# Kernel tuning notes

Hardware: AMD Instinct MI355X
Metric: run time of the kernel (lower is better)

## Reference

```python
import jax, jax.numpy as jnp
import numpy as np

N_NODES = 100000


def gcn_conv(x, W, b, src, dst, n_nodes):
    """PyG-style GCNConv: out = D^{-1/2} (A + I) D^{-1/2} (x @ W) + b."""
    h = x @ W  # [N, F_out] transform first (smaller message dim)
    # add self-loops
    loops = jnp.arange(n_nodes, dtype=src.dtype)
    s = jnp.concatenate([src, loops])
    d = jnp.concatenate([dst, loops])
    # symmetric normalization
    deg = jnp.zeros((n_nodes,), dtype=h.dtype).at[d].add(1.0)
    dinv = jnp.where(deg > 0, jax.lax.rsqrt(deg), 0.0)
    norm = dinv[s] * dinv[d]  # [E+N]
    msg = h[s] * norm[:, None]  # gather from sources
    out = jax.ops.segment_sum(msg, d, num_segments=n_nodes)  # scatter-add at targets
    return out + b


def setup_inputs() -> dict:
    key = jax.random.key(0)
    k1, k2, k3, k4 = jax.random.split(key, 4)
    in_ch, hid, out_ch = 128, 75, 40
    n_edges = 3200000
    x = jax.random.normal(k1, (N_NODES, in_ch), dtype=jnp.float32)
    edge_index = jax.random.randint(k2, (2, n_edges), 0, N_NODES, dtype=jnp.int64)
    # Glorot-style init for GCNConv weights, zero bias (PyG default)
    W1 = jax.random.normal(k3, (in_ch, hid), dtype=jnp.float32) * (1.0 / np.sqrt(in_ch))
    b1 = jnp.zeros((hid,), dtype=jnp.float32)
    W2 = jax.random.normal(k4, (hid, out_ch), dtype=jnp.float32) * (1.0 / np.sqrt(hid))
    b2 = jnp.zeros((out_ch,), dtype=jnp.float32)
    return {"x": x, "edge_index": edge_index, "W1": W1, "b1": b1, "W2": W2, "b2": b2}


def reference(x, edge_index, W1, b1, W2, b2):
    src, dst = edge_index[0], edge_index[1]
    h = gcn_conv(x, W1, b1, src, dst, N_NODES)
    h = jax.nn.relu(h)
    h = gcn_conv(h, W2, b2, src, dst, N_NODES)
    return jax.nn.log_softmax(h, axis=1)
```

## Files before the change

kernel.cpp:

```cpp
#include <hip/hip_runtime.h>

#define N_NODES 100000
#define IN_CH 128
#define HID 75
#define OUT_CH 40
#define N_EDGES 3200000

#define NB 196
#define CAP 20000
#define EPT 16
#define PA_EDGES (EPT * 256)

typedef unsigned short u16;
typedef unsigned int u32;
typedef unsigned char u8;
typedef short short8 __attribute__((ext_vector_type(8)));
typedef float f32x4 __attribute__((ext_vector_type(4)));
typedef float f32x2 __attribute__((ext_vector_type(2)));
typedef u32 u32x2 __attribute__((ext_vector_type(2)));
typedef u32 u32x4 __attribute__((ext_vector_type(4)));

__device__ __forceinline__ u16 f2bf(float f) {
    u32 b = __float_as_uint(f);
    b += 0x7FFF + ((b >> 16) & 1);
    return (u16)(b >> 16);
}

#if __has_builtin(__builtin_amdgcn_cvt_pk_f32_fp8) && __has_builtin(__builtin_amdgcn_cvt_pk_fp8_f32)
#define HW_FP8 1
#else
#define HW_FP8 0
#endif

__device__ __forceinline__ float dec1_sw(u32 v) {
    u32 s = (v & 0x80u) << 24;
    u32 em = v & 0x7Fu;
    float mag = (em >= 8u) ? __uint_as_float((em << 20) + (120u << 23))
                           : (float)em * 0.001953125f;
    return __uint_as_float(s | __float_as_uint(mag));
}
template <int HI>
__device__ __forceinline__ f32x2 dec2(u32 w) {
#if HW_FP8
    return __builtin_amdgcn_cvt_pk_f32_fp8(w, HI);
#else
    f32x2 r;
    r.x = dec1_sw((w >> (HI * 16)) & 0xFFu);
    r.y = dec1_sw((w >> (HI * 16 + 8)) & 0xFFu);
    return r;
#endif
}
__device__ __forceinline__ u32 enc1(float f) {
#if HW_FP8
    return __builtin_amdgcn_cvt_pk_fp8_f32(f, f, 0u, false) & 0xFFu;
#else
    float cf = fminf(fmaxf(f, -448.f), 448.f);
    u32 b = __float_as_uint(cf);
    u32 sign = (b >> 24) & 0x80u;
    float af = fabsf(cf);
    if (af < 0.015625f) {
        u32 d = (u32)__builtin_rintf(af * 512.f);
        return sign | d;
    }
    u32 e = (b >> 23) & 0xFFu;
    u32 m = b & 0x7FFFFFu;
    u32 m8 = m >> 20;
    u32 rem = m & 0xFFFFFu;
    m8 += (rem > 0x80000u) || (rem == 0x80000u && (m8 & 1u));
    u32 ee = e - 120u;
    if (m8 == 8u) { m8 = 0u; ee += 1u; }
    if (ee > 15u || (ee == 15u && m8 == 7u)) { ee = 15u; m8 = 6u; }
    return sign | (ee << 3) | m8;
#endif
}

__global__ void probe64(const int* __restrict__ e, int* __restrict__ flag) {
    __shared__ int nonzero;
    if (threadIdx.x == 0) nonzero = 0;
    __syncthreads();
    int idx = threadIdx.x * 12497;
    if (e[2 * idx + 1] != 0) nonzero = 1;
    __syncthreads();
    if (threadIdx.x == 0) *flag = (nonzero == 0) ? 1 : 0;
}

__global__ __launch_bounds__(256) void init_misc(int* __restrict__ bucketCursor,
        u32* __restrict__ h1b32) {
    int i = blockIdx.x * 256 + threadIdx.x;
    if (i < NB * 16) bucketCursor[i] = 0;
    if (i < 800000) {
        int node = i >> 3, q = i & 7;
        h1b32[node * 48 + 40 + q] = 0;
    }
}

__global__ __launch_bounds__(256) void passA(const int* __restrict__ e,
        const int* __restrict__ flag, int* __restrict__ bucketCursor,
        unsigned* __restrict__ bucketBuf) {
    __shared__ int cnt[NB];
    __shared__ int base[NB];
    int t = threadIdx.x;
    for (int i = t; i < NB; i += 256) cnt[i] = 0;
    __syncthreads();
    bool w64 = (*flag != 0);
    int s_[EPT], d_[EPT];
    int eb = blockIdx.x * PA_EDGES + t;
#pragma unroll
    for (int k = 0; k < EPT; ++k) {
        int idx = eb + k * 256;
        int s = 0, d = -1;
        if (idx < N_EDGES) {
            if (w64) { s = e[2 * idx]; d = e[2 * (N_EDGES + idx)]; }
            else     { s = e[idx];     d = e[N_EDGES + idx]; }
            atomicAdd(&cnt[d >> 9], 1);
        }
        s_[k] = s; d_[k] = d;
    }
    __syncthreads();
    for (int i = t; i < NB; i += 256) {
        int c = cnt[i];
        base[i] = (c > 0) ? atomicAdd(&bucketCursor[i * 16], c) : 0;
        cnt[i] = 0;
    }
    __syncthreads();
#pragma unroll
    for (int k = 0; k < EPT; ++k) {
        int d = d_[k];
        if (d >= 0) {
            int b = d >> 9;
            int off = atomicAdd(&cnt[b], 1);
            int pos = base[b] + off;
            if (pos < CAP)
                bucketBuf[(size_t)b * CAP + pos] =
                    ((unsigned)(d & 511) << 17) | (unsigned)s_[k];
        }
    }
}

__global__ __launch_bounds__(256) void scan196(const int* __restrict__ bucketCursor,
        int* __restrict__ bucketStart, int* __restrict__ rowStart) {
    __shared__ int a[256], b[256];
    int t = threadIdx.x;
    int v = (t < NB) ? bucketCursor[t * 16] : 0;
    a[t] = v;
    __syncthreads();
    int* pin = a; int* pout = b;
    for (int o = 1; o < 256; o <<= 1) {
        int nv = pin[t] + ((t >= o) ? pin[t - o] : 0);
        pout[t] = nv;
        __syncthreads();
        int* tmp = pin; pin = pout; pout = tmp;
    }
    if (t < NB) bucketStart[t] = pin[t] - v;
    if (t == 0) rowStart[N_NODES] = N_EDGES;
}

__global__ __launch_bounds__(1024) void passB(const unsigned* __restrict__ bucketBuf,
        const int* __restrict__ bucketCursor, const int* __restrict__ bucketStart,
        int* __restrict__ csrSrc, int* __restrict__ rowStart, float* __restrict__ dinv) {
    __shared__ int cnt[512];
    __shared__ int sa[512], sb[512];
    int b = blockIdx.x;
    int t = threadIdx.x;
    int n = bucketCursor[b * 16];
    int start = bucketStart[b];
    if (t < 512) cnt[t] = 0;
    __syncthreads();
    const unsigned* buf = bucketBuf + (size_t)b * CAP;
    for (int i = t; i < n; i += 1024) atomicAdd(&cnt[buf[i] >> 17], 1);
    __syncthreads();
    if (t < 512) sa[t] = cnt[t];
    __syncthreads();
    int* pin = sa; int* pout = sb;
    for (int o = 1; o < 512; o <<= 1) {
        if (t < 512) pout[t] = pin[t] + ((t >= o) ? pin[t - o] : 0);
        __syncthreads();
        int* tmp = pin; pin = pout; pout = tmp;
    }
    int excl = 0;
    if (t < 512) {
        int deg = cnt[t];
        excl = pin[t] - deg;
        int node = b * 512 + t;
        if (node < N_NODES) {
            rowStart[node] = start + excl;
            dinv[node] = rsqrtf((float)deg + 1.0f);
        }
    }
    __syncthreads();
    if (t < 512) cnt[t] = excl;
    __syncthreads();
    for (int i = t; i < n; i += 1024) {
        unsigned p = buf[i];
        int pos = atomicAdd(&cnt[p >> 17], 1);
        csrSrc[start + pos] = (int)(p & 0x1FFFF);
    }
}

__global__ __launch_bounds__(256) void prep_w(const float* __restrict__ W1,
        const float* __restrict__ W2, u16* __restrict__ w1t, u16* __restrict__ w2t) {
    int g = blockIdx.x * 256 + threadIdx.x;
    int stride = gridDim.x * 256;
    for (int i = g; i < 80 * 128; i += stride) {
        int c = i >> 7, k = i & 127;
        w1t[i] = (c < HID) ? f2bf(W1[k * HID + c]) : (u16)0;
    }
    for (int i = g; i < 48 * 96; i += stride) {
        int c = i / 96, k = i - c * 96;
        w2t[i] = (c < OUT_CH && k < HID) ? f2bf(W2[k * OUT_CH + c]) : (u16)0;
    }
}

__global__ __launch_bounds__(256) void gemm1_mfma(const float* __restrict__ x,
        const u16* __restrict__ w1t, const float* __restrict__ dinv,
        u8* __restrict__ hsA8, u8* __restrict__ hsB8) {
    __shared__ u16 Wl[80 * 136];
    int t = threadIdx.x;
    {
        const u32* ws = (const u32*)w1t;
        u32* wd = (u32*)Wl;
        for (int i = t; i < 80 * 64; i += 256) {
            int r = i >> 6, c = i & 63;
            wd[r * 68 + c] = ws[i];
        }
    }
    __syncthreads();
    int wid = t >> 6, lane = t & 63;
    int bl = lane & 15, kh = lane >> 4;
    int row0 = blockIdx.x * 64 + wid * 16;
    short8 bf[5][4];
#pragma unroll
    for (int ct = 0; ct < 5; ++ct)
#pragma unroll
        for (int ks = 0; ks < 4; ++ks)
            bf[ct][ks] = *(const short8*)&Wl[(ct * 16 + bl) * 136 + ks * 32 + kh * 8];
    f32x4 zero = {0.f, 0.f, 0.f, 0.f};
    f32x4 acc[5];
#pragma unroll
    for (int ct = 0; ct < 5; ++ct) acc[ct] = zero;
    int arow = row0 + bl;
    bool av = (arow < N_NODES);
    const float* xr = x + (size_t)arow * IN_CH + kh * 8;
#pragma unroll
    for (int ks = 0; ks < 4; ++ks) {
        short8 af = {0, 0, 0, 0, 0, 0, 0, 0};
        if (av) {
            float4 lo = *(const float4*)(xr + ks * 32);
            float4 hi = *(const float4*)(xr + ks * 32 + 4);
            af[0] = (short)f2bf(lo.x); af[1] = (short)f2bf(lo.y);
            af[2] = (short)f2bf(lo.z); af[3] = (short)f2bf(lo.w);
            af[4] = (short)f2bf(hi.x); af[5] = (short)f2bf(hi.y);
            af[6] = (short)f2bf(hi.z); af[7] = (short)f2bf(hi.w);
        }
#pragma unroll
        for (int ct = 0; ct < 5; ++ct)
            acc[ct] = __builtin_amdgcn_mfma_f32_16x16x32_bf16(af, bf[ct][ks], acc[ct], 0, 0, 0);
    }
    int orow = row0 + kh * 4;
    float dn[4];
#pragma unroll
    for (int i = 0; i < 4; ++i)
        dn[i] = (orow + i < N_NODES) ? dinv[orow + i] * 8.f : 0.f;
#pragma unroll
    for (int ct = 0; ct < 5; ++ct) {
        int col = ct * 16 + bl;
#pragma unroll
        for (int i = 0; i < 4; ++i) {
            int r = orow + i;
            if (r < N_NODES) {
                u8 q8 = (u8)enc1(acc[ct][i] * dn[i]);
                if (ct < 4) hsA8[(size_t)r * 64 + col] = q8;
                else        hsB8[(size_t)r * 16 + (col - 64)] = q8;
            }
        }
    }
}

__global__ __launch_bounds__(256) void gemm2_mfma(const u16* __restrict__ h1b,
        const u16* __restrict__ w2t, const float* __restrict__ dinv,
        u8* __restrict__ hs2A8, u8* __restrict__ hs2B8) {
    __shared__ u16 Wl[48 * 104];
    int t = threadIdx.x;
    {
        const u32* ws = (const u32*)w2t;
        u32* wd = (u32*)Wl;
        for (int i = t; i < 48 * 48; i += 256) {
            int r = i / 48, c = i - r * 48;
            wd[r * 52 + c] = ws[i];
        }
    }
    __syncthreads();
    int wid = t >> 6, lane = t & 63;
    int bl = lane & 15, kh = lane >> 4;
    int row0 = blockIdx.x * 64 + wid * 16;
    short8 bf[3][3];
#pragma unroll
    for (int ct = 0; ct < 3; ++ct)
#pragma unroll
        for (int ks = 0; ks < 3; ++ks)
            bf[ct][ks] = *(const short8*)&Wl[(ct * 16 + bl) * 104 + ks * 32 + kh * 8];
    f32x4 zero = {0.f, 0.f, 0.f, 0.f};
    f32x4 acc[3];
#pragma unroll
    for (int ct = 0; ct < 3; ++ct) acc[ct] = zero;
    int arow = row0 + bl;
    bool av = (arow < N_NODES);
    const u16* hr = h1b + (size_t)arow * 96 + kh * 8;
#pragma unroll
    for (int ks = 0; ks < 3; ++ks) {
        short8 af = {0, 0, 0, 0, 0, 0, 0, 0};
        if (av) af = *(const short8*)(hr + ks * 32);
#pragma unroll
        for (int ct = 0; ct < 3; ++ct)
            acc[ct] = __builtin_amdgcn_mfma_f32_16x16x32_bf16(af, bf[ct][ks], acc[ct], 0, 0, 0);
    }
    int orow = row0 + kh * 4;
    float dn[4];
#pragma unroll
    for (int i = 0; i < 4; ++i)
        dn[i] = (orow + i < N_NODES) ? dinv[orow + i] * 8.f : 0.f;
#pragma unroll
    for (int ct = 0; ct < 3; ++ct) {
        int col = ct * 16 + bl;
#pragma unroll
        for (int i = 0; i < 4; ++i) {
            int r = orow + i;
            if (r < N_NODES) {
                u8 q8 = (u8)enc1(acc[ct][i] * dn[i]);
                if (ct < 2)      hs2A8[(size_t)r * 32 + col] = q8;
                else if (bl < 8) hs2B8[(size_t)r * 8 + (col - 32)] = q8;
            }
        }
    }
}

__global__ __launch_bounds__(256) void aggregate1(
        const char* __restrict__ tab, int delta1,
        const int* __restrict__ rowStart, const int* __restrict__ csrSrc,
        const float* __restrict__ dinv, const float* __restrict__ bias,
        u32* __restrict__ out) {
    int wid = threadIdx.x >> 6, lane = threadIdx.x & 63;
    int node = __builtin_amdgcn_readfirstlane(blockIdx.x * 4 + wid);
    if (node >= N_NODES) return;
    int g = lane / 10;
    int ll = lane - 10 * g;
    bool isB = ll >= 8;
    u32 loff = isB ? (u32)(ll - 8) * 8 + (u32)delta1 : (u32)ll * 8;
    int sh = isB ? 4 : 6;
    bool act = lane < 60;
    f32x2 a0 = {0.f, 0.f}, a1 = {0.f, 0.f}, a2 = {0.f, 0.f}, a3 = {0.f, 0.f};
    if (lane < 10) {
        u32x2 v = *(const u32x2*)(tab + (((u32)node << sh) + loff));
        a0 += dec2<0>(v.x); a1 += dec2<1>(v.x);
        a2 += dec2<0>(v.y); a3 += dec2<1>(v.y);
    }
    int j = rowStart[node], end = rowStart[node + 1];
    for (; j + 24 <= end; j += 24) {
        u32 iv[4]; u32x2 vv[4];
#pragma unroll
        for (int q = 0; q < 4; ++q) iv[q] = act ? (u32)csrSrc[j + 6 * q + g] : 0u;
#pragma unroll
        for (int q = 0; q < 4; ++q) {
            u32x2 z = {0u, 0u};
            vv[q] = act ? *(const u32x2*)(tab + ((iv[q] << sh) + loff)) : z;
        }
#pragma unroll
        for (int q = 0; q < 4; ++q) {
            a0 += dec2<0>(vv[q].x); a1 += dec2<1>(vv[q].x);
            a2 += dec2<0>(vv[q].y); a3 += dec2<1>(vv[q].y);
        }
    }
    for (; j < end; j += 6) {
        bool p = act && (j + g < end);
        u32 ivx = p ? (u32)csrSrc[j + g] : 0u;
        u32x2 z = {0u, 0u};
        u32x2 v = p ? *(const u32x2*)(tab + ((ivx << sh) + loff)) : z;
        a0 += dec2<0>(v.x); a1 += dec2<1>(v.x);
        a2 += dec2<0>(v.y); a3 += dec2<1>(v.y);
    }
    float tt[8] = {a0.x, a0.y, a1.x, a1.y, a2.x, a2.y, a3.x, a3.y};
#pragma unroll
    for (int k = 0; k < 8; ++k) {
        tt[k] += __shfl(tt[k], lane + 30);
        tt[k] += __shfl(tt[k], lane + 10) + __shfl(tt[k], lane + 20);
    }
    if (lane < 10) {
        float dns = dinv[node] * 0.125f;
        u32x4 ov;
#pragma unroll
        for (int k = 0; k < 4; ++k) {
            int f0 = 8 * ll + 2 * k;
            float rlo = (f0 < HID) ? fmaxf(fmaf(dns, tt[2 * k], bias[f0]), 0.f) : 0.f;
            float rhi = (f0 + 1 < HID) ? fmaxf(fmaf(dns, tt[2 * k + 1], bias[f0 + 1]), 0.f) : 0.f;
            ov[k] = ((u32)f2bf(rhi) << 16) | (u32)f2bf(rlo);
        }
        *(u32x4*)(out + (size_t)node * 48 + 4 * ll) = ov;
    }
}

__global__ __launch_bounds__(256) void aggregate2(
        const char* __restrict__ tab, int delta2,
        const int* __restrict__ rowStart, const int* __restrict__ csrSrc,
        const float* __restrict__ dinv, const float* __restrict__ bias,
        float* __restrict__ out) {
    int wid = threadIdx.x >> 6, lane = threadIdx.x & 63;
    int node = __builtin_amdgcn_readfirstlane(blockIdx.x * 4 + wid);
    if (node >= N_NODES) return;
    int g = lane / 5;
    int ll = lane - 5 * g;
    bool isB = (ll == 4);
    u32 loff = isB ? (u32)delta2 : (u32)ll * 8;
    int sh = isB ? 3 : 5;
    bool act = lane < 60;
    f32x2 a0 = {0.f, 0.f}, a1 = {0.f, 0.f}, a2 = {0.f, 0.f}, a3 = {0.f, 0.f};
    if (lane < 5) {
        u32x2 v = *(const u32x2*)(tab + (((u32)node << sh) + loff));
        a0 += dec2<0>(v.x); a1 += dec2<1>(v.x);
        a2 += dec2<0>(v.y); a3 += dec2<1>(v.y);
    }
    int j = rowStart[node], end = rowStart[node + 1];
    for (; j + 24 <= end; j += 24) {
        u32 iv[2]; u32x2 vv[2];
#pragma unroll
        for (int q = 0; q < 2; ++q) iv[q] = act ? (u32)csrSrc[j + 12 * q + g] : 0u;
#pragma unroll
        for (int q = 0; q < 2; ++q) {
            u32x2 z = {0u, 0u};
            vv[q] = act ? *(const u32x2*)(tab + ((iv[q] << sh) + loff)) : z;
        }
#pragma unroll
        for (int q = 0; q < 2; ++q) {
            a0 += dec2<0>(vv[q].x); a1 += dec2<1>(vv[q].x);
            a2 += dec2<0>(vv[q].y); a3 += dec2<1>(vv[q].y);
        }
    }
    for (; j < end; j += 12) {
        bool p = act && (j + g < end);
        u32 ivx = p ? (u32)csrSrc[j + g] : 0u;
        u32x2 z = {0u, 0u};
        u32x2 v = p ? *(const u32x2*)(tab + ((ivx << sh) + loff)) : z;
        a0 += dec2<0>(v.x); a1 += dec2<1>(v.x);
        a2 += dec2<0>(v.y); a3 += dec2<1>(v.y);
    }
    float tt[8] = {a0.x, a0.y, a1.x, a1.y, a2.x, a2.y, a3.x, a3.y};
#pragma unroll
    for (int k = 0; k < 8; ++k) {
        tt[k] += __shfl(tt[k], lane + 30);
        tt[k] += __shfl(tt[k], lane + 10) + __shfl(tt[k], lane + 20);
        tt[k] += __shfl(tt[k], lane + 5);
    }
    bool act5 = lane < 5;
    float vk[8];
    float m = -3.4e38f;
    if (act5) {
        float dns = dinv[node] * 0.125f;
#pragma unroll
        for (int k = 0; k < 8; ++k) {
            vk[k] = fmaf(dns, tt[k], bias[8 * ll + k]);
            m = fmaxf(m, vk[k]);
        }
    }
#pragma unroll
    for (int o = 1; o < 8; o <<= 1) m = fmaxf(m, __shfl_xor(m, o));
    float e = 0.f;
    if (act5) {
#pragma unroll
        for (int k = 0; k < 8; ++k) e += expf(vk[k] - m);
    }
#pragma unroll
    for (int o = 1; o < 8; o <<= 1) e += __shfl_xor(e, o);
    float lse = logf(e);
    if (act5) {
        float4 r0 = make_float4(vk[0] - m - lse, vk[1] - m - lse,
                                vk[2] - m - lse, vk[3] - m - lse);
        float4 r1 = make_float4(vk[4] - m - lse, vk[5] - m - lse,
                                vk[6] - m - lse, vk[7] - m - lse);
        *(float4*)(out + (size_t)node * OUT_CH + 8 * ll) = r0;
        *(float4*)(out + (size_t)node * OUT_CH + 8 * ll + 4) = r1;
    }
}

extern "C" void kernel_launch(void* const* d_in, const int* in_sizes, int n_in,
                              void* d_out, int out_size, void* d_ws, size_t ws_size,
                              hipStream_t stream) {
    const float* x  = (const float*)d_in[0];
    const int*   e  = (const int*)d_in[1];
    const float* W1 = (const float*)d_in[2];
    const float* b1 = (const float*)d_in[3];
    const float* W2 = (const float*)d_in[4];
    const float* b2 = (const float*)d_in[5];
    float* out = (float*)d_out;

    char* w = (char*)d_ws;
    u8* hsA8 = (u8*)w;
    u8* hsB8 = (u8*)(w + 6402048);
    unsigned* bucketBuf = (unsigned*)w;
    w += 15680000;
    u16* h1b  = (u16*)w; w += (size_t)100032 * 96 * 2;
    int* csrSrc = (int*)w; w += (size_t)N_EDGES * 4;
    u8* hs2A8 = (u8*)w; w += (size_t)100032 * 32;
    u8* hs2B8 = (u8*)w; w += (size_t)100032 * 8;
    int* rowStart = (int*)w; w += 400016;
    float* dinv   = (float*)w; w += 400000;
    int* bucketCursor = (int*)w; w += NB * 16 * 4;
    int* bucketStart  = (int*)w; w += 1024;
    u16* w1t = (u16*)w; w += 80 * 128 * 2;
    u16* w2t = (u16*)w; w += 48 * 96 * 2;
    int* flag = (int*)w; w += 16;

    int delta1 = (int)((char*)hsB8 - (char*)hsA8);
    int delta2 = (int)((char*)hs2B8 - (char*)hs2A8);

    probe64<<<1, 256, 0, stream>>>(e, flag);
    init_misc<<<3126, 256, 0, stream>>>(bucketCursor, (u32*)h1b);
    passA<<<(N_EDGES + PA_EDGES - 1) / PA_EDGES, 256, 0, stream>>>(
        e, flag, bucketCursor, bucketBuf);
    scan196<<<1, 256, 0, stream>>>(bucketCursor, bucketStart, rowStart);
    passB<<<NB, 1024, 0, stream>>>(bucketBuf, bucketCursor, bucketStart,
                                   csrSrc, rowStart, dinv);
    prep_w<<<16, 256, 0, stream>>>(W1, W2, w1t, w2t);

    gemm1_mfma<<<(N_NODES + 63) / 64, 256, 0, stream>>>(x, w1t, dinv, hsA8, hsB8);
    aggregate1<<<(N_NODES + 3) / 4, 256, 0, stream>>>(
        (const char*)hsA8, delta1, rowStart, csrSrc, dinv, b1, (u32*)h1b);
    gemm2_mfma<<<(N_NODES + 63) / 64, 256, 0, stream>>>(h1b, w2t, dinv, hs2A8, hs2B8);
    aggregate2<<<(N_NODES + 3) / 4, 256, 0, stream>>>(
        (const char*)hs2A8, delta2, rowStart, csrSrc, dinv, b2, out);
}
```

Baseline: 264.4 us.

## Widen aggregate1 gathers to 16B and pad layer-2 table to 64B rows

aggregate1 now assigns 5 lanes per edge, each loading 16 bytes, so 12 edges are processed per wave step instead of 6 with 8-byte loads. The layer-2 quantized features move from a split A/B table into a single padded table with 64-byte rows, which removes the per-lane branch and delta offset in aggregate2. The goal is fewer memory instructions per gathered row and simpler addressing. In exchange the layer-2 table takes more memory footprint per node, and aggregate1 holds more accumulator registers.

```diff
diff --git a/kernel.cpp b/kernel.cpp
--- a/kernel.cpp
+++ b/kernel.cpp
@@ -278,7 +278,7 @@
 
 __global__ __launch_bounds__(256) void gemm2_mfma(const u16* __restrict__ h1b,
         const u16* __restrict__ w2t, const float* __restrict__ dinv,
-        u8* __restrict__ hs2A8, u8* __restrict__ hs2B8) {
+        u8* __restrict__ hs2P) {
     __shared__ u16 Wl[48 * 104];
     int t = threadIdx.x;
     {
@@ -325,10 +325,9 @@
 #pragma unroll
         for (int i = 0; i < 4; ++i) {
             int r = orow + i;
-            if (r < N_NODES) {
+            if (r < N_NODES && (ct < 2 || bl < 8)) {
                 u8 q8 = (u8)enc1(acc[ct][i] * dn[i]);
-                if (ct < 2)      hs2A8[(size_t)r * 32 + col] = q8;
-                else if (bl < 8) hs2B8[(size_t)r * 8 + (col - 32)] = q8;
+                hs2P[(size_t)r * 64 + col] = q8;
             }
         }
     }
@@ -342,64 +341,77 @@
     int wid = threadIdx.x >> 6, lane = threadIdx.x & 63;
     int node = __builtin_amdgcn_readfirstlane(blockIdx.x * 4 + wid);
     if (node >= N_NODES) return;
-    int g = lane / 10;
-    int ll = lane - 10 * g;
-    bool isB = ll >= 8;
-    u32 loff = isB ? (u32)(ll - 8) * 8 + (u32)delta1 : (u32)ll * 8;
+    int g = lane / 5;
+    int ll = lane - 5 * g;
+    bool isB = (ll == 4);
+    u32 loff = isB ? (u32)delta1 : (u32)ll * 16;
     int sh = isB ? 4 : 6;
     bool act = lane < 60;
-    f32x2 a0 = {0.f, 0.f}, a1 = {0.f, 0.f}, a2 = {0.f, 0.f}, a3 = {0.f, 0.f};
-    if (lane < 10) {
-        u32x2 v = *(const u32x2*)(tab + (((u32)node << sh) + loff));
-        a0 += dec2<0>(v.x); a1 += dec2<1>(v.x);
-        a2 += dec2<0>(v.y); a3 += dec2<1>(v.y);
+    f32x2 acc[8];
+#pragma unroll
+    for (int k = 0; k < 8; ++k) { acc[k].x = 0.f; acc[k].y = 0.f; }
+    if (lane < 5) {
+        u32x4 v = *(const u32x4*)(tab + (((u32)node << sh) + loff));
+        acc[0] += dec2<0>(v.x); acc[1] += dec2<1>(v.x);
+        acc[2] += dec2<0>(v.y); acc[3] += dec2<1>(v.y);
+        acc[4] += dec2<0>(v.z); acc[5] += dec2<1>(v.z);
+        acc[6] += dec2<0>(v.w); acc[7] += dec2<1>(v.w);
     }
     int j = rowStart[node], end = rowStart[node + 1];
     for (; j + 24 <= end; j += 24) {
-        u32 iv[4]; u32x2 vv[4];
-#pragma unroll
-        for (int q = 0; q < 4; ++q) iv[q] = act ? (u32)csrSrc[j + 6 * q + g] : 0u;
-#pragma unroll
-        for (int q = 0; q < 4; ++q) {
-            u32x2 z = {0u, 0u};
-            vv[q] = act ? *(const u32x2*)(tab + ((iv[q] << sh) + loff)) : z;
-        }
-#pragma unroll
-        for (int q = 0; q < 4; ++q) {
-            a0 += dec2<0>(vv[q].x); a1 += dec2<1>(vv[q].x);
-            a2 += dec2<0>(vv[q].y); a3 += dec2<1>(vv[q].y);
-        }
-    }
-    for (; j < end; j += 6) {
+        u32 iv[2]; u32x4 vv[2];
+#pragma unroll
+        for (int q = 0; q < 2; ++q) iv[q] = act ? (u32)csrSrc[j + 12 * q + g] : 0u;
+#pragma unroll
+        for (int q = 0; q < 2; ++q) {
+            u32x4 z = {0u, 0u, 0u, 0u};
+            vv[q] = act ? *(const u32x4*)(tab + ((iv[q] << sh) + loff)) : z;
+        }
+#pragma unroll
+        for (int q = 0; q < 2; ++q) {
+            acc[0] += dec2<0>(vv[q].x); acc[1] += dec2<1>(vv[q].x);
+            acc[2] += dec2<0>(vv[q].y); acc[3] += dec2<1>(vv[q].y);
+            acc[4] += dec2<0>(vv[q].z); acc[5] += dec2<1>(vv[q].z);
+            acc[6] += dec2<0>(vv[q].w); acc[7] += dec2<1>(vv[q].w);
+        }
+    }
+    for (; j < end; j += 12) {
         bool p = act && (j + g < end);
         u32 ivx = p ? (u32)csrSrc[j + g] : 0u;
-        u32x2 z = {0u, 0u};
-        u32x2 v = p ? *(const u32x2*)(tab + ((ivx << sh) + loff)) : z;
-        a0 += dec2<0>(v.x); a1 += dec2<1>(v.x);
-        a2 += dec2<0>(v.y); a3 += dec2<1>(v.y);
-    }
-    float tt[8] = {a0.x, a0.y, a1.x, a1.y, a2.x, a2.y, a3.x, a3.y};
-#pragma unroll
-    for (int k = 0; k < 8; ++k) {
+        u32x4 z = {0u, 0u, 0u, 0u};
+        u32x4 v = p ? *(const u32x4*)(tab + ((ivx << sh) + loff)) : z;
+        acc[0] += dec2<0>(v.x); acc[1] += dec2<1>(v.x);
+        acc[2] += dec2<0>(v.y); acc[3] += dec2<1>(v.y);
+        acc[4] += dec2<0>(v.z); acc[5] += dec2<1>(v.z);
+        acc[6] += dec2<0>(v.w); acc[7] += dec2<1>(v.w);
+    }
+    float tt[16];
+#pragma unroll
+    for (int k = 0; k < 8; ++k) { tt[2 * k] = acc[k].x; tt[2 * k + 1] = acc[k].y; }
+#pragma unroll
+    for (int k = 0; k < 16; ++k) {
         tt[k] += __shfl(tt[k], lane + 30);
         tt[k] += __shfl(tt[k], lane + 10) + __shfl(tt[k], lane + 20);
-    }
-    if (lane < 10) {
+        tt[k] += __shfl(tt[k], lane + 5);
+    }
+    if (lane < 5) {
         float dns = dinv[node] * 0.125f;
-        u32x4 ov;
-#pragma unroll
-        for (int k = 0; k < 4; ++k) {
-            int f0 = 8 * ll + 2 * k;
+        u32x4 o0, o1;
+#pragma unroll
+        for (int k = 0; k < 8; ++k) {
+            int f0 = 16 * lane + 2 * k;
             float rlo = (f0 < HID) ? fmaxf(fmaf(dns, tt[2 * k], bias[f0]), 0.f) : 0.f;
             float rhi = (f0 + 1 < HID) ? fmaxf(fmaf(dns, tt[2 * k + 1], bias[f0 + 1]), 0.f) : 0.f;
-            ov[k] = ((u32)f2bf(rhi) << 16) | (u32)f2bf(rlo);
-        }
-        *(u32x4*)(out + (size_t)node * 48 + 4 * ll) = ov;
+            u32 wd = ((u32)f2bf(rhi) << 16) | (u32)f2bf(rlo);
+            if (k < 4) o0[k] = wd; else o1[k - 4] = wd;
+        }
+        *(u32x4*)(out + (size_t)node * 48 + 8 * lane) = o0;
+        *(u32x4*)(out + (size_t)node * 48 + 8 * lane + 4) = o1;
     }
 }
 
 __global__ __launch_bounds__(256) void aggregate2(
-        const char* __restrict__ tab, int delta2,
+        const char* __restrict__ tab,
         const int* __restrict__ rowStart, const int* __restrict__ csrSrc,
         const float* __restrict__ dinv, const float* __restrict__ bias,
         float* __restrict__ out) {
@@ -408,13 +420,11 @@
     if (node >= N_NODES) return;
     int g = lane / 5;
     int ll = lane - 5 * g;
-    bool isB = (ll == 4);
-    u32 loff = isB ? (u32)delta2 : (u32)ll * 8;
-    int sh = isB ? 3 : 5;
+    u32 loff = (u32)ll * 8;
     bool act = lane < 60;
     f32x2 a0 = {0.f, 0.f}, a1 = {0.f, 0.f}, a2 = {0.f, 0.f}, a3 = {0.f, 0.f};
     if (lane < 5) {
-        u32x2 v = *(const u32x2*)(tab + (((u32)node << sh) + loff));
+        u32x2 v = *(const u32x2*)(tab + (((u32)node << 6) + loff));
         a0 += dec2<0>(v.x); a1 += dec2<1>(v.x);
         a2 += dec2<0>(v.y); a3 += dec2<1>(v.y);
     }
@@ -426,7 +436,7 @@
 #pragma unroll
         for (int q = 0; q < 2; ++q) {
             u32x2 z = {0u, 0u};
-            vv[q] = act ? *(const u32x2*)(tab + ((iv[q] << sh) + loff)) : z;
+            vv[q] = act ? *(const u32x2*)(tab + ((iv[q] << 6) + loff)) : z;
         }
 #pragma unroll
         for (int q = 0; q < 2; ++q) {
@@ -438,7 +448,7 @@
         bool p = act && (j + g < end);
         u32 ivx = p ? (u32)csrSrc[j + g] : 0u;
         u32x2 z = {0u, 0u};
-        u32x2 v = p ? *(const u32x2*)(tab + ((ivx << sh) + loff)) : z;
+        u32x2 v = p ? *(const u32x2*)(tab + ((ivx << 6) + loff)) : z;
         a0 += dec2<0>(v.x); a1 += dec2<1>(v.x);
         a2 += dec2<0>(v.y); a3 += dec2<1>(v.y);
     }
@@ -498,8 +508,7 @@
     w += 15680000;
     u16* h1b  = (u16*)w; w += (size_t)100032 * 96 * 2;
     int* csrSrc = (int*)w; w += (size_t)N_EDGES * 4;
-    u8* hs2A8 = (u8*)w; w += (size_t)100032 * 32;
-    u8* hs2B8 = (u8*)w; w += (size_t)100032 * 8;
+    u8* hs2P = (u8*)w; w += (size_t)100032 * 64;
     int* rowStart = (int*)w; w += 400016;
     float* dinv   = (float*)w; w += 400000;
     int* bucketCursor = (int*)w; w += NB * 16 * 4;
@@ -509,7 +518,6 @@
     int* flag = (int*)w; w += 16;
 
     int delta1 = (int)((char*)hsB8 - (char*)hsA8);
-    int delta2 = (int)((char*)hs2B8 - (char*)hs2A8);
 
     probe64<<<1, 256, 0, stream>>>(e, flag);
     init_misc<<<3126, 256, 0, stream>>>(bucketCursor, (u32*)h1b);
@@ -523,7 +531,7 @@
     gemm1_mfma<<<(N_NODES + 63) / 64, 256, 0, stream>>>(x, w1t, dinv, hsA8, hsB8);
     aggregate1<<<(N_NODES + 3) / 4, 256, 0, stream>>>(
         (const char*)hsA8, delta1, rowStart, csrSrc, dinv, b1, (u32*)h1b);
-    gemm2_mfma<<<(N_NODES + 63) / 64, 256, 0, stream>>>(h1b, w2t, dinv, hs2A8, hs2B8);
+    gemm2_mfma<<<(N_NODES + 63) / 64, 256, 0, stream>>>(h1b, w2t, dinv, hs2P);
     aggregate2<<<(N_NODES + 3) / 4, 256, 0, stream>>>(
-        (const char*)hs2A8, delta2, rowStart, csrSrc, dinv, b2, out);
-}
+        (const char*)hs2P, rowStart, csrSrc, dinv, b2, out);
+}
```

Measured after the change: 257.6 us. 2.6% less time.
